# Kernel optimization log

Hardware: AMD Instinct MI355X
Metric: run time of the kernel (lower is better)

Reference implementation:

```python
import jax, jax.numpy as jnp
import numpy as np

B, T, H = 64, 512, 1024

def setup_inputs() -> dict:
    key = jax.random.key(0)
    ks = jax.random.split(key, 6)
    scale = 1.0 / np.sqrt(H)
    return {
        "s_t": jax.random.normal(ks[0], (B, H), dtype=jnp.float32),
        "prev_s": jax.random.normal(ks[1], (B, T, H), dtype=jnp.float32),
        "W_prev": jax.random.normal(ks[2], (H, H), dtype=jnp.float32) * scale,
        "W_s": jax.random.normal(ks[3], (H, H), dtype=jnp.float32) * scale,
        "b_s": jax.random.normal(ks[4], (H,), dtype=jnp.float32) * scale,
        "v": jax.random.normal(ks[5], (H,), dtype=jnp.float32) * scale,
    }

def reference(s_t, prev_s, W_prev, W_s, b_s, v):
    # et = W_prev(prev_s)                       [B,T,H]
    et = jnp.einsum('bth,oh->bto', prev_s, W_prev)
    # dec_fea = W_s(s_t).unsqueeze(1)           [B,1,H]
    dec_fea = (jnp.einsum('bh,oh->bo', s_t, W_s) + b_s)[:, None, :]
    # scores = v(tanh(et + dec_fea)).squeeze    [B,T]
    scores = jnp.einsum('bth,h->bt', jnp.tanh(et + dec_fea), v)
    at = jax.nn.softmax(scores, axis=1)         # [B,T]
    ct_d = jnp.einsum('bt,bth->bh', at, prev_s)  # bmm(at[:,None,:], prev_s).squeeze(1)
    new_prev_s = jnp.concatenate([prev_s, s_t[:, None, :]], axis=1)  # [B,T+1,H]
    return ct_d, new_prev_s
```

## Files before the change

kernel.cpp:

```cpp
#include <hip/hip_runtime.h>
#include <hip/hip_bf16.h>

#define B_DIM 64
#define T_DIM 512
#define H_DIM 1024

typedef __attribute__((ext_vector_type(4))) float f32x4;

#define AQ8_OFF  0UL
#define BQ8_OFF  33554432UL
#define DEC_OFF  34603008UL
#define PART_OFF 34865152UL
#define AT_OFF   35913728UL

__device__ __forceinline__ unsigned cvt4_fp8(float a, float b, float c, float d) {
  unsigned r = 0;
  r = __builtin_amdgcn_cvt_pk_fp8_f32(a, b, r, false);
  r = __builtin_amdgcn_cvt_pk_fp8_f32(c, d, r, true);
  return r;
}

__device__ __forceinline__ void gload_lds16(const void* g, void* l) {
  __builtin_amdgcn_global_load_lds(
      (const __attribute__((address_space(1))) void*)g,
      (__attribute__((address_space(3))) void*)l, 16, 0, 0);
}


__global__ __launch_bounds__(256) void prep_ws(
    const float* __restrict__ prev,
    const float* __restrict__ st,
    const float* __restrict__ Wp,
    const float* __restrict__ Ws,
    const float* __restrict__ bs,
    float* __restrict__ out,
    unsigned char* __restrict__ Aq,
    unsigned char* __restrict__ Wq,
    float* __restrict__ dec) {
  __shared__ unsigned char lq[2][16][528];
  int bid = blockIdx.x;
  int tid = threadIdx.x;

  if (bid < 256) {
    int lane = tid & 63, w = tid >> 6;
    int o = bid * 4 + w;
    const float4* wrow = (const float4*)(Ws + (size_t)o * H_DIM);
    float4 w0 = wrow[lane], w1 = wrow[64 + lane],
           w2 = wrow[128 + lane], w3 = wrow[192 + lane];
    const float4* st4 = (const float4*)st;
    float bias = bs[o];
    #pragma unroll 8
    for (int b = 0; b < B_DIM; b++) {
      const float4* s = st4 + (size_t)b * 256;
      float4 s0 = s[lane], s1 = s[64 + lane], s2 = s[128 + lane], s3 = s[192 + lane];
      float p = w0.x * s0.x + w0.y * s0.y + w0.z * s0.z + w0.w * s0.w
              + w1.x * s1.x + w1.y * s1.y + w1.z * s1.z + w1.w * s1.w
              + w2.x * s2.x + w2.y * s2.y + w2.z * s2.z + w2.w * s2.w
              + w3.x * s3.x + w3.y * s3.y + w3.z * s3.z + w3.w * s3.w;
      p += __shfl_xor(p, 1);  p += __shfl_xor(p, 2);
      p += __shfl_xor(p, 4);  p += __shfl_xor(p, 8);
      p += __shfl_xor(p, 16); p += __shfl_xor(p, 32);
      if (lane == 0) dec[(size_t)b * H_DIM + o] = p + bias;
    }
  } else if (bid < 2368) {
    bool isA = bid < 2304;
    int mt = isA ? bid - 256 : bid - 2304;
    const f32x4* src4 = (const f32x4*)(isA ? prev : Wp) + (size_t)mt * 4096;
    f32x4* dst4 = nullptr;
    if (isA) {
      int b = mt >> 5, t0 = (mt & 31) * 16;
      dst4 = (f32x4*)out + 16384 + (size_t)b * 131328 + (size_t)t0 * 256;
    }
    unsigned char* q8 = (isA ? Aq : Wq) + (size_t)mt * 16384;
    float scale = isA ? 4.f : 16.f;

    f32x4 buf[8];
    #pragma unroll
    for (int p = 0; p < 8; p++) {
      int idx = p * 256 + tid;
      int r = idx >> 7, cg = idx & 127;
      buf[p] = src4[(size_t)r * 256 + cg];
    }
    #pragma unroll
    for (int p = 0; p < 8; p++) {
      int idx = p * 256 + tid;
      int r = idx >> 7, cg = idx & 127;
      if (isA) dst4[(size_t)r * 256 + cg] = buf[p];
      *(unsigned*)&lq[0][r][cg * 4] =
          cvt4_fp8(buf[p][0] * scale, buf[p][1] * scale,
                   buf[p][2] * scale, buf[p][3] * scale);
    }
    #pragma unroll
    for (int p = 0; p < 8; p++) {
      int idx = p * 256 + tid;
      int r = idx >> 7, cg = idx & 127;
      buf[p] = src4[(size_t)r * 256 + 128 + cg];
    }
    asm volatile("s_waitcnt lgkmcnt(0)" ::: "memory");
    __builtin_amdgcn_s_barrier();

    #pragma unroll
    for (int cc = 0; cc < 2; cc++) {
      int c = cc * 256 + tid;
      int ktl = c >> 5, ci = c & 31;
      int r0 = (2 * ci) & 15, oct = ci >> 3;
      uint2 lo = *(const uint2*)&lq[0][r0][ktl * 32 + oct * 8];
      uint2 hi = *(const uint2*)&lq[0][r0 + 1][ktl * 32 + oct * 8];
      uint4 val = make_uint4(lo.x, lo.y, hi.x, hi.y);
      *(uint4*)(q8 + (size_t)ktl * 512 + ci * 16) = val;
    }
    #pragma unroll
    for (int p = 0; p < 8; p++) {
      int idx = p * 256 + tid;
      int r = idx >> 7, cg = idx & 127;
      if (isA) dst4[(size_t)r * 256 + 128 + cg] = buf[p];
      *(unsigned*)&lq[1][r][cg * 4] =
          cvt4_fp8(buf[p][0] * scale, buf[p][1] * scale,
                   buf[p][2] * scale, buf[p][3] * scale);
    }
    asm volatile("s_waitcnt lgkmcnt(0)" ::: "memory");
    __builtin_amdgcn_s_barrier();

    #pragma unroll
    for (int cc = 0; cc < 2; cc++) {
      int c = cc * 256 + tid;
      int ktl = c >> 5, ci = c & 31;
      int r0 = (2 * ci) & 15, oct = ci >> 3;
      uint2 lo = *(const uint2*)&lq[1][r0][ktl * 32 + oct * 8];
      uint2 hi = *(const uint2*)&lq[1][r0 + 1][ktl * 32 + oct * 8];
      uint4 val = make_uint4(lo.x, lo.y, hi.x, hi.y);
      *(uint4*)(q8 + (size_t)(16 + ktl) * 512 + ci * 16) = val;
    }
  } else {
    const f32x4* s4 = (const f32x4*)st;
    for (int b = 0; b < B_DIM; b++) {
      f32x4* o4 = (f32x4*)out + 16384 + (size_t)b * 131328 + 131072;
      o4[tid] = s4[(size_t)b * 256 + tid];
    }
  }
}

__global__ __launch_bounds__(256, 3) void score_gemm(
    const unsigned char* __restrict__ Aq,
    const unsigned char* __restrict__ Bq,
    const float* __restrict__ dec,
    const float* __restrict__ v,
    float* __restrict__ part)
{
  __shared__ __align__(16) unsigned char ldsA[2][8192];
  __shared__ __align__(16) unsigned char ldsB[2][8192];

  int orig = blockIdx.x;
  int swz = (orig & 7) * 256 + (orig >> 3);
  int bm = swz >> 3, bn = swz & 7;

  int tid = threadIdx.x;
  int lane = tid & 63, w = tid >> 6;
  int wm = w >> 1, wn = w & 1;
  size_t m0 = (size_t)bm * 128;

  f32x4 acc[4][4];
  #pragma unroll
  for (int i = 0; i < 4; i++)
    #pragma unroll
    for (int j = 0; j < 4; j++) {
      f32x4 z; z[0] = 0.f; z[1] = 0.f; z[2] = 0.f; z[3] = 0.f;
      acc[i][j] = z;
    }

  int fA = tid >> 5, cif = tid & 31;
  const unsigned char* aSrc0 =
      Aq + ((size_t)(bm * 8 + (fA >> 1)) * 32 + (fA & 1)) * 512 + (size_t)cif * 16;
  const unsigned char* aSrc1 =
      Aq + ((size_t)(bm * 8 + (fA >> 1) + 4) * 32 + (fA & 1)) * 512 + (size_t)cif * 16;
  const unsigned char* bSrc0 =
      Bq + ((size_t)(bn * 8 + (fA >> 1)) * 32 + (fA & 1)) * 512 + (size_t)cif * 16;
  const unsigned char* bSrc1 =
      Bq + ((size_t)(bn * 8 + (fA >> 1) + 4) * 32 + (fA & 1)) * 512 + (size_t)cif * 16;

#define STAGE(buf, t) do { \
    size_t ko = (size_t)(t) * 1024; \
    gload_lds16(aSrc0 + ko, &ldsA[(buf)][tid * 16]); \
    gload_lds16(aSrc1 + ko, &ldsA[(buf)][tid * 16 + 4096]); \
    gload_lds16(bSrc0 + ko, &ldsB[(buf)][tid * 16]); \
    gload_lds16(bSrc1 + ko, &ldsB[(buf)][tid * 16 + 4096]); \
  } while (0)

  STAGE(0, 0);

  #pragma unroll 2
  for (int t = 0; t < 16; t++) {
    int cur = t & 1, nxt = cur ^ 1;
    if (t < 15) {
      STAGE(nxt, t + 1);
      asm volatile("s_waitcnt vmcnt(4)" ::: "memory");
    } else {
      asm volatile("s_waitcnt vmcnt(0)" ::: "memory");
    }
    __builtin_amdgcn_s_barrier();
    asm volatile("" ::: "memory");

    const unsigned char* Ac = &ldsA[cur][0];
    const unsigned char* Bc = &ldsB[cur][0];
    long av[4][2], bv[4][2];
    #pragma unroll
    for (int mf = 0; mf < 4; mf++)
      #pragma unroll
      for (int kk = 0; kk < 2; kk++)
        av[mf][kk] = *(const long*)(Ac + ((wm * 4 + mf) * 2 + kk) * 512 + lane * 8);
    #pragma unroll
    for (int nf = 0; nf < 4; nf++)
      #pragma unroll
      for (int kk = 0; kk < 2; kk++)
        bv[nf][kk] = *(const long*)(Bc + ((wn * 4 + nf) * 2 + kk) * 512 + lane * 8);

    __builtin_amdgcn_s_setprio(1);
    #pragma unroll
    for (int kk = 0; kk < 2; kk++)
      #pragma unroll
      for (int mf = 0; mf < 4; mf++)
        #pragma unroll
        for (int nf = 0; nf < 4; nf++)
          acc[mf][nf] = __builtin_amdgcn_mfma_f32_16x16x32_fp8_fp8(
              av[mf][kk], bv[nf][kk], acc[mf][nf], 0, 0, 0);
    __builtin_amdgcn_s_setprio(0);
    asm volatile("" ::: "memory");
    __builtin_amdgcn_s_barrier();
  }
#undef STAGE

  int b = (int)(m0 >> 9);
  int lr = lane >> 4, lc = lane & 15;
  int n0 = bn * 128;
  float dv[4], vv[4];
  #pragma unroll
  for (int nf = 0; nf < 4; nf++) {
    int col = n0 + wn * 64 + nf * 16 + lc;
    dv[nf] = dec[(size_t)b * H_DIM + col];
    vv[nf] = v[col];
  }
  float* epi = (float*)&ldsA[0][0];
  #pragma unroll
  for (int mf = 0; mf < 4; mf++) {
    #pragma unroll
    for (int r = 0; r < 4; r++) {
      float s = 0.f;
      #pragma unroll
      for (int nf = 0; nf < 4; nf++) {
        float x = acc[mf][nf][r] * 0.015625f + dv[nf];
        x = fminf(fmaxf(x, -15.f), 15.f);
        float e = __expf(2.f * x);
        s += vv[nf] * (e - 1.f) * __builtin_amdgcn_rcpf(e + 1.f);
      }
      s += __shfl_xor(s, 1); s += __shfl_xor(s, 2);
      s += __shfl_xor(s, 4); s += __shfl_xor(s, 8);
      if (lc == 0) epi[(wm * 64 + mf * 16 + lr * 4 + r) * 2 + wn] = s;
    }
  }
  __syncthreads();
  if (tid < 128) {
    part[(m0 + tid) * 8 + bn] = epi[tid * 2] + epi[tid * 2 + 1];
  }
}

__global__ void softmax_kernel(const float* __restrict__ part, float* __restrict__ at) {
  int b = blockIdx.x, tid = threadIdx.x;
  __shared__ float sc[512];
  __shared__ float red[8];
  #pragma unroll
  for (int rep = 0; rep < 2; rep++) {
    int t = rep * 256 + tid;
    const float* p = part + ((size_t)b * 512 + t) * 8;
    sc[t] = p[0] + p[1] + p[2] + p[3] + p[4] + p[5] + p[6] + p[7];
  }
  __syncthreads();
  float m = fmaxf(sc[tid], sc[tid + 256]);
  for (int d = 1; d < 64; d <<= 1) m = fmaxf(m, __shfl_xor(m, d));
  if ((tid & 63) == 0) red[tid >> 6] = m;
  __syncthreads();
  m = fmaxf(fmaxf(red[0], red[1]), fmaxf(red[2], red[3]));
  float e0 = __expf(sc[tid] - m), e1 = __expf(sc[tid + 256] - m);
  float s = e0 + e1;
  for (int d = 1; d < 64; d <<= 1) s += __shfl_xor(s, d);
  if ((tid & 63) == 0) red[4 + (tid >> 6)] = s;
  __syncthreads();
  s = red[4] + red[5] + red[6] + red[7];
  float inv = 1.f / s;
  at[(size_t)b * 512 + tid] = e0 * inv;
  at[(size_t)b * 512 + tid + 256] = e1 * inv;
}

__global__ void ctd_ws(const unsigned char* __restrict__ Aq,
                       const float* __restrict__ at, float* __restrict__ out) {
  int wid = blockIdx.x * 4 + (threadIdx.x >> 6);
  int lane = threadIdx.x & 63;
  int b = wid >> 5, kt = wid & 31;
  int lc = lane & 15, lr = lane >> 4;
  float a8[8] = {0.f, 0.f, 0.f, 0.f, 0.f, 0.f, 0.f, 0.f};
  const unsigned char* base =
      Aq + ((size_t)b * 32 * 32 + kt) * 512 + (size_t)lane * 8;
  const float* atb = at + (size_t)b * 512;
  #pragma unroll 8
  for (int mt = 0; mt < 32; mt++) {
    float a = atb[mt * 16 + lc];
    uint2 uv = *(const uint2*)(base + (size_t)mt * 16384);
    a8[0] += a * __builtin_amdgcn_cvt_f32_fp8(uv.x, 0);
    a8[1] += a * __builtin_amdgcn_cvt_f32_fp8(uv.x, 1);
    a8[2] += a * __builtin_amdgcn_cvt_f32_fp8(uv.x, 2);
    a8[3] += a * __builtin_amdgcn_cvt_f32_fp8(uv.x, 3);
    a8[4] += a * __builtin_amdgcn_cvt_f32_fp8(uv.y, 0);
    a8[5] += a * __builtin_amdgcn_cvt_f32_fp8(uv.y, 1);
    a8[6] += a * __builtin_amdgcn_cvt_f32_fp8(uv.y, 2);
    a8[7] += a * __builtin_amdgcn_cvt_f32_fp8(uv.y, 3);
  }
  #pragma unroll
  for (int d = 1; d < 16; d <<= 1)
    #pragma unroll
    for (int j = 0; j < 8; j++) a8[j] += __shfl_xor(a8[j], d);
  if (lc == 0) {
    #pragma unroll
    for (int j = 0; j < 8; j++)
      out[(size_t)b * H_DIM + kt * 32 + lr * 8 + j] = a8[j] * 0.25f;
  }
}

extern "C" void kernel_launch(void* const* d_in, const int* in_sizes, int n_in,
                              void* d_out, int out_size, void* d_ws, size_t ws_size,
                              hipStream_t stream) {
  (void)in_sizes; (void)n_in; (void)out_size; (void)ws_size;
  const float* s_t    = (const float*)d_in[0];
  const float* prev_s = (const float*)d_in[1];
  const float* W_prev = (const float*)d_in[2];
  const float* W_s    = (const float*)d_in[3];
  const float* b_s    = (const float*)d_in[4];
  const float* v      = (const float*)d_in[5];
  float* out = (float*)d_out;
  char* ws = (char*)d_ws;

  unsigned char* Aq = (unsigned char*)(ws + AQ8_OFF);
  unsigned char* Wq = (unsigned char*)(ws + BQ8_OFF);
  float* dec  = (float*)(ws + DEC_OFF);
  float* part = (float*)(ws + PART_OFF);
  float* at   = (float*)(ws + AT_OFF);

  prep_ws<<<2369, 256, 0, stream>>>(prev_s, s_t, W_prev, W_s, b_s, out, Aq, Wq, dec);
  score_gemm<<<2048, 256, 0, stream>>>(Aq, Wq, dec, v, part);
  softmax_kernel<<<64, 256, 0, stream>>>(part, at);
  ctd_ws<<<512, 256, 0, stream>>>(Aq, at, out);
}
```

Measured before the change: 149.1 us.

## Split prev_s copy into separate blocks and fuse softmax into context kernel

The prep kernel now gives the fp32 copy of prev_s into the output its own blocks, interleaved with the fp8 quantization blocks, instead of doing both in one block. This raises parallelism and shortens the critical path per block. Softmax is folded into the ctd kernel: each of the 8 blocks per batch recomputes the softmax from the partial scores into shared memory, which removes one launch and the round trip of the at array through global memory. The cost is redundant softmax work (8x per batch) and twice as many prep blocks, each re-reading prev_s.

```diff
diff --git a/kernel.cpp b/kernel.cpp
--- a/kernel.cpp
+++ b/kernel.cpp
@@ -62,15 +62,24 @@
       p += __shfl_xor(p, 16); p += __shfl_xor(p, 32);
       if (lane == 0) dec[(size_t)b * H_DIM + o] = p + bias;
     }
-  } else if (bid < 2368) {
-    bool isA = bid < 2304;
-    int mt = isA ? bid - 256 : bid - 2304;
+  } else if (bid < 4352 && ((bid - 256) & 1)) {
+    int mt = (bid - 256) >> 1;
+    const f32x4* src4 = (const f32x4*)prev + (size_t)mt * 4096;
+    int b = mt >> 5, t0 = (mt & 31) * 16;
+    f32x4* dst4 = (f32x4*)out + 16384 + (size_t)b * 131328 + (size_t)t0 * 256;
+    f32x4 cb[8];
+    #pragma unroll
+    for (int p = 0; p < 8; p++) cb[p] = src4[p * 256 + tid];
+    #pragma unroll
+    for (int p = 0; p < 8; p++) dst4[p * 256 + tid] = cb[p];
+    #pragma unroll
+    for (int p = 0; p < 8; p++) cb[p] = src4[2048 + p * 256 + tid];
+    #pragma unroll
+    for (int p = 0; p < 8; p++) dst4[2048 + p * 256 + tid] = cb[p];
+  } else if (bid < 4416) {
+    bool isA = bid < 4352;
+    int mt = isA ? ((bid - 256) >> 1) : (bid - 4352);
     const f32x4* src4 = (const f32x4*)(isA ? prev : Wp) + (size_t)mt * 4096;
-    f32x4* dst4 = nullptr;
-    if (isA) {
-      int b = mt >> 5, t0 = (mt & 31) * 16;
-      dst4 = (f32x4*)out + 16384 + (size_t)b * 131328 + (size_t)t0 * 256;
-    }
     unsigned char* q8 = (isA ? Aq : Wq) + (size_t)mt * 16384;
     float scale = isA ? 4.f : 16.f;
 
@@ -85,7 +94,6 @@
     for (int p = 0; p < 8; p++) {
       int idx = p * 256 + tid;
       int r = idx >> 7, cg = idx & 127;
-      if (isA) dst4[(size_t)r * 256 + cg] = buf[p];
       *(unsigned*)&lq[0][r][cg * 4] =
           cvt4_fp8(buf[p][0] * scale, buf[p][1] * scale,
                    buf[p][2] * scale, buf[p][3] * scale);
@@ -113,7 +121,6 @@
     for (int p = 0; p < 8; p++) {
       int idx = p * 256 + tid;
       int r = idx >> 7, cg = idx & 127;
-      if (isA) dst4[(size_t)r * 256 + 128 + cg] = buf[p];
       *(unsigned*)&lq[1][r][cg * 4] =
           cvt4_fp8(buf[p][0] * scale, buf[p][1] * scale,
                    buf[p][2] * scale, buf[p][3] * scale);
@@ -263,10 +270,17 @@
   }
 }
 
-__global__ void softmax_kernel(const float* __restrict__ part, float* __restrict__ at) {
-  int b = blockIdx.x, tid = threadIdx.x;
+__global__ __launch_bounds__(256) void ctd_ws(
+    const unsigned char* __restrict__ Aq,
+    const float* __restrict__ part,
+    float* __restrict__ out) {
   __shared__ float sc[512];
   __shared__ float red[8];
+  __shared__ float at_l[512];
+  int blk = blockIdx.x;
+  int tid = threadIdx.x;
+  int b = blk >> 3;
+
   #pragma unroll
   for (int rep = 0; rep < 2; rep++) {
     int t = rep * 256 + tid;
@@ -286,23 +300,19 @@
   __syncthreads();
   s = red[4] + red[5] + red[6] + red[7];
   float inv = 1.f / s;
-  at[(size_t)b * 512 + tid] = e0 * inv;
-  at[(size_t)b * 512 + tid + 256] = e1 * inv;
-}
-
-__global__ void ctd_ws(const unsigned char* __restrict__ Aq,
-                       const float* __restrict__ at, float* __restrict__ out) {
-  int wid = blockIdx.x * 4 + (threadIdx.x >> 6);
-  int lane = threadIdx.x & 63;
-  int b = wid >> 5, kt = wid & 31;
+  at_l[tid] = e0 * inv;
+  at_l[tid + 256] = e1 * inv;
+  __syncthreads();
+
+  int lane = tid & 63, w = tid >> 6;
+  int kt = (blk & 7) * 4 + w;
   int lc = lane & 15, lr = lane >> 4;
   float a8[8] = {0.f, 0.f, 0.f, 0.f, 0.f, 0.f, 0.f, 0.f};
   const unsigned char* base =
-      Aq + ((size_t)b * 32 * 32 + kt) * 512 + (size_t)lane * 8;
-  const float* atb = at + (size_t)b * 512;
+      Aq + ((size_t)b * 1024 + kt) * 512 + (size_t)lane * 8;
   #pragma unroll 8
   for (int mt = 0; mt < 32; mt++) {
-    float a = atb[mt * 16 + lc];
+    float a = at_l[mt * 16 + lc];
     uint2 uv = *(const uint2*)(base + (size_t)mt * 16384);
     a8[0] += a * __builtin_amdgcn_cvt_f32_fp8(uv.x, 0);
     a8[1] += a * __builtin_amdgcn_cvt_f32_fp8(uv.x, 1);
@@ -341,10 +351,8 @@
   unsigned char* Wq = (unsigned char*)(ws + BQ8_OFF);
   float* dec  = (float*)(ws + DEC_OFF);
   float* part = (float*)(ws + PART_OFF);
-  float* at   = (float*)(ws + AT_OFF);
-
-  prep_ws<<<2369, 256, 0, stream>>>(prev_s, s_t, W_prev, W_s, b_s, out, Aq, Wq, dec);
+
+  prep_ws<<<4417, 256, 0, stream>>>(prev_s, s_t, W_prev, W_s, b_s, out, Aq, Wq, dec);
   score_gemm<<<2048, 256, 0, stream>>>(Aq, Wq, dec, v, part);
-  softmax_kernel<<<64, 256, 0, stream>>>(part, at);
-  ctd_ws<<<512, 256, 0, stream>>>(Aq, at, out);
-}
+  ctd_ws<<<512, 256, 0, stream>>>(Aq, part, out);
+}
```

Result: no change. 148.0 us (-0.7%).
